# Performance work log

Hardware: AMD Instinct MI355X
Metric: run time of the kernel (lower is better)

The kernel has to match this reference:

```python
import jax, jax.numpy as jnp
import numpy as np
import math

N_HEADS = 16
D_EMB = 1024
D_HEAD = D_EMB // N_HEADS


def setup_inputs() -> dict:
    key = jax.random.key(0)
    ks = jax.random.split(key, 5)
    scale_in = 1.0 / math.sqrt(D_EMB)
    x = jax.random.normal(ks[0], (2, 2048, D_EMB), dtype=jnp.float32)
    w_in = jax.random.uniform(ks[1], (3 * D_EMB, D_EMB), dtype=jnp.float32, minval=-scale_in, maxval=scale_in)
    b_in = jax.random.uniform(ks[2], (3 * D_EMB,), dtype=jnp.float32, minval=-scale_in, maxval=scale_in)
    w_out = jax.random.uniform(ks[3], (D_EMB, D_EMB), dtype=jnp.float32, minval=-scale_in, maxval=scale_in)
    b_out = jax.random.uniform(ks[4], (D_EMB,), dtype=jnp.float32, minval=-scale_in, maxval=scale_in)
    return {"x": x, "w_in": w_in, "b_in": b_in, "w_out": w_out, "b_out": b_out, "apply_mask": 1}


def reference(x, w_in, b_in, w_out, b_out, apply_mask):
    B, S, D = x.shape
    # fused QKV projection: torch Linear uses y = x @ W^T + b
    qkv = jnp.einsum('bsd,ed->bse', x, w_in) + b_in  # [B,S,3D]
    q, k, v = jnp.split(qkv, 3, axis=-1)
    # [B,H,S,Dh]
    q = q.reshape(B, S, N_HEADS, D_HEAD).transpose(0, 2, 1, 3)
    k = k.reshape(B, S, N_HEADS, D_HEAD).transpose(0, 2, 1, 3)
    v = v.reshape(B, S, N_HEADS, D_HEAD).transpose(0, 2, 1, 3)
    w = jnp.einsum('bhqd,bhkd->bhqk', q, k)  # [B,H,S,S]
    if apply_mask:
        causal = jnp.triu(jnp.ones((S, S), dtype=bool), k=1)
        w = jnp.where(causal, -jnp.inf, w)
    w = w / jnp.sqrt(jnp.float32(D_HEAD)).astype(w.dtype)
    w = jax.nn.softmax(w, axis=-1)
    score = jnp.einsum('bhqk,bhkd->bhqd', w, v)  # [B,H,S,Dh]
    score = score.transpose(0, 2, 1, 3).reshape(B, S, D)
    return jnp.einsum('bsd,ed->bse', score, w_out) + b_out
```

## Files before the change

kernel.cpp:

```cpp
#include <hip/hip_runtime.h>
#include <stdint.h>

#define DEMB 1024
#define NHEAD 16
#define DHEAD 64
#define SEQ 2048
#define MROWS 4096

typedef __bf16 bf16x8 __attribute__((ext_vector_type(8)));
typedef float f32x4 __attribute__((ext_vector_type(4)));
typedef unsigned short u16;

#define LOG2E 1.44269504088896340736f

__device__ __forceinline__ u16 f2b(float f) {
  return __builtin_bit_cast(u16, (__bf16)f);
}
__device__ __forceinline__ uint32_t pk2(float a, float b) {
  return (uint32_t)f2b(a) | ((uint32_t)f2b(b) << 16);
}

__device__ __forceinline__ f32x4 mfma16(bf16x8 a, bf16x8 b, f32x4 c) {
  return __builtin_amdgcn_mfma_f32_16x16x32_bf16(a, b, c, 0, 0, 0);
}

__device__ __forceinline__ void gload_lds16(const void* g, void* l) {
  __builtin_amdgcn_global_load_lds(
      (__attribute__((address_space(1))) unsigned int*)(g),
      (__attribute__((address_space(3))) unsigned int*)(l), 16, 0, 0);
}

__device__ __forceinline__ void tile_barrier() {
  __builtin_amdgcn_sched_barrier(0);
  asm volatile("s_waitcnt vmcnt(0) lgkmcnt(0)" ::: "memory");
  __builtin_amdgcn_s_barrier();
  __builtin_amdgcn_sched_barrier(0);
}

__global__ void cvt3_f32_bf16(const float* __restrict__ a, int na,
                              const float* __restrict__ b, int nb,
                              const float* __restrict__ c, int nc,
                              u16* __restrict__ da, u16* __restrict__ db,
                              u16* __restrict__ dc) {
  const int total = (na + nb + nc) >> 2;
  const int stride = gridDim.x * blockDim.x;
  for (int t = blockIdx.x * blockDim.x + threadIdx.x; t < total; t += stride) {
    int i = t << 2;
    const float* s;
    u16* d;
    if (i < na) {
      s = a + i; d = da + i;
    } else if (i < na + nb) {
      s = b + (i - na); d = db + (i - na);
    } else {
      s = c + (i - na - nb); d = dc + (i - na - nb);
    }
    float4 f = *(const float4*)s;
    ushort4 o;
    o.x = f2b(f.x); o.y = f2b(f.y); o.z = f2b(f.z); o.w = f2b(f.w);
    *(ushort4*)d = o;
  }
}

template <int EPI>
__global__ __launch_bounds__(256, 2) void gemm_nt(
    const u16* __restrict__ A, const u16* __restrict__ Bw,
    const float* __restrict__ bias, int K, int N,
    u16* __restrict__ q_out, u16* __restrict__ k_out, u16* __restrict__ v_out,
    float* __restrict__ f_out) {
  __shared__ __align__(16) u16 As[128 * 64];
  __shared__ __align__(16) u16 Bs[128 * 64];
  const int tid = threadIdx.x;
  const int w = tid >> 6;
  const int lane = tid & 63;
  const int wm = w >> 1, wn = w & 1;
  const int m0 = blockIdx.y * 128, n0 = blockIdx.x * 128;
  const int l16 = lane & 15, lg = lane >> 4;
  const int st_row = lane >> 3, st_slot = lane & 7;

  f32x4 acc[4][4] = {};

  for (int k0 = 0; k0 < K; k0 += 64) {
#pragma unroll
    for (int i = 0; i < 4; ++i) {
      const int chunk = (w << 2) | i;
      const int row = (chunk << 3) | st_row;
      const int scol = (st_slot ^ (row & 7)) << 3;
      gload_lds16(A + (size_t)(m0 + row) * K + k0 + scol, (char*)As + (chunk << 10));
      gload_lds16(Bw + (size_t)(n0 + row) * K + k0 + scol, (char*)Bs + (chunk << 10));
    }
    __syncthreads();
#pragma unroll
    for (int ks = 0; ks < 2; ++ks) {
      bf16x8 af[4], bfr[4];
#pragma unroll
      for (int mi = 0; mi < 4; ++mi) {
        const int row = wm * 64 + mi * 16 + l16;
        const int cb = ((ks << 6) | (lg << 4)) ^ ((row & 7) << 4);
        af[mi] = *(const bf16x8*)((const char*)As + row * 128 + cb);
      }
#pragma unroll
      for (int ni = 0; ni < 4; ++ni) {
        const int row = wn * 64 + ni * 16 + l16;
        const int cb = ((ks << 6) | (lg << 4)) ^ ((row & 7) << 4);
        bfr[ni] = *(const bf16x8*)((const char*)Bs + row * 128 + cb);
      }
#pragma unroll
      for (int mi = 0; mi < 4; ++mi)
#pragma unroll
        for (int ni = 0; ni < 4; ++ni)
          acc[mi][ni] = mfma16(af[mi], bfr[ni], acc[mi][ni]);
    }
    __syncthreads();
  }

#pragma unroll
  for (int ni = 0; ni < 4; ++ni) {
    const int n = n0 + wn * 64 + ni * 16 + l16;
    const float bv = bias[n];
    if (EPI == 0) {
      const int part = n >> 10;
      const int hh = (n >> 6) & 15;
      const int dh = n & 63;
      if (part == 2) {
#pragma unroll
        for (int mi = 0; mi < 4; ++mi) {
          const int mbase = m0 + wm * 64 + mi * 16 + (lg << 2);
          const int bq = mbase >> 11, s0 = mbase & 2047;
          ushort4 o;
          o.x = f2b(acc[mi][ni][0] + bv);
          o.y = f2b(acc[mi][ni][1] + bv);
          o.z = f2b(acc[mi][ni][2] + bv);
          o.w = f2b(acc[mi][ni][3] + bv);
          *(ushort4*)(v_out + ((size_t)(((bq << 4) | hh) * 64 + dh)) * SEQ + s0) = o;
        }
      } else {
        const float scl = (part == 0) ? (0.125f * LOG2E) : 1.0f;
        u16* dst = (part == 0) ? q_out : k_out;
#pragma unroll
        for (int mi = 0; mi < 4; ++mi) {
#pragma unroll
          for (int i = 0; i < 4; ++i) {
            const int m = m0 + wm * 64 + mi * 16 + (lg << 2) + i;
            const int bq = m >> 11, s = m & 2047;
            dst[((size_t)((bq << 4) | hh) * SEQ + s) * DHEAD + dh] = f2b((acc[mi][ni][i] + bv) * scl);
          }
        }
      }
    } else {
#pragma unroll
      for (int mi = 0; mi < 4; ++mi)
#pragma unroll
        for (int i = 0; i < 4; ++i) {
          const int m = m0 + wm * 64 + mi * 16 + (lg << 2) + i;
          f_out[(size_t)m * N + n] = acc[mi][ni][i] + bv;
        }
    }
  }
}

__device__ __forceinline__ int swz4(int r) { return (r ^ (r >> 3)) & 15; }

__device__ __forceinline__ void stage_k(const u16* __restrict__ Kb, size_t base,
                                        int jt, u16* Ks, int w, int lane) {
#pragma unroll
  for (int i = 0; i < 4; ++i) {
    const int g = (w << 2) | i;
    const int row = (g << 2) | (lane >> 4);
    const int shat = (lane & 15) ^ swz4(row);
    const int kv = (row << 1) | (shat >> 3);
    const int del = (shat & 7) << 3;
    gload_lds16(Kb + base + (size_t)(jt * 128 + kv) * DHEAD + del,
                (char*)Ks + (g << 10));
  }
}

__device__ __forceinline__ void stage_v(const u16* __restrict__ VTg, size_t base,
                                        int jt, u16* Vs, int w, int lane) {
#pragma unroll
  for (int i = 0; i < 4; ++i) {
    const int g = (w << 2) | i;
    const int row = (g << 2) | (lane >> 4);
    const int shat = (lane & 15) ^ swz4(row);
    gload_lds16(VTg + base + (size_t)row * SEQ + jt * 128 + (shat << 3),
                (char*)Vs + (g << 10));
  }
}

__global__ __launch_bounds__(256, 2) void attn_fwd(
    const u16* __restrict__ Qb, const u16* __restrict__ Kb,
    const u16* __restrict__ VTg, u16* __restrict__ Ob,
    const int* __restrict__ amask) {
  __shared__ __align__(16) u16 Ks[2][64 * 128];
  __shared__ __align__(16) u16 Vt[2][64 * 128];
  __shared__ __align__(16) uint32_t Ps[4][1024];
  const int tid = threadIdx.x;
  const int w = tid >> 6, lane = tid & 63;
  const int l16 = lane & 15, lg = lane >> 4;

  const int id = blockIdx.x;
  const int xcd = id & 7;
  const int r = id >> 3;
  const int bh = (xcd << 2) | (r & 3);
  const int p = r >> 2;
  const int qiA = 31 - p, qiB = p;

  const size_t base = (size_t)bh * (SEQ * DHEAD);
  const bool causal = (amask[0] != 0);
  const int ntA = causal ? ((qiA >> 1) + 1) : (SEQ / 128);
  const int ntB = causal ? ((qiB >> 1) + 1) : (SEQ / 128);
  const int nt = ntA + ntB;
  const int b = bh >> 4, h = bh & 15;

  int qseg0 = qiA * 64;

  bf16x8 qf[2];
  {
    const u16* qp = Qb + base + (size_t)(qseg0 + (w << 4) + l16) * DHEAD + (lg << 3);
    qf[0] = *(const bf16x8*)qp;
    qf[1] = *(const bf16x8*)(qp + 32);
  }

  float mrow = -1e30f, lrowp = 0.f;
  f32x4 oacc[4] = {};

  const int key = (l16 & 7) << 2;
  char* prow = (char*)(&Ps[w][0]) + l16 * 256;

  stage_k(Kb, base, 0, Ks[0], w, lane);
  stage_v(VTg, base, 0, Vt[0], w, lane);
  tile_barrier();

  int cur = 0;
  for (int t = 0; t < nt; ++t) {
    const int j = (t >= ntA) ? (t - ntA) : t;
    const u16* Kcur = Ks[cur];
    const u16* Vcur = Vt[cur];
    const bool pre = (t + 1 < nt);
    const int jn = (t + 1 >= ntA) ? (t + 1 - ntA) : (t + 1);
    if (pre) stage_k(Kb, base, jn, Ks[cur ^ 1], w, lane);

    f32x4 sv[8];
    __builtin_amdgcn_s_setprio(1);
#pragma unroll
    for (int nf = 0; nf < 8; ++nf) {
      const int row2 = (nf << 3) | (l16 >> 1);
      const int sz = swz4(row2);
      const int s0 = ((l16 & 1) << 3) | lg;
      bf16x8 kf0 = *(const bf16x8*)((const char*)Kcur + row2 * 256 + ((s0 ^ sz) << 4));
      bf16x8 kf1 = *(const bf16x8*)((const char*)Kcur + row2 * 256 + (((s0 | 4) ^ sz) << 4));
      f32x4 s = {};
      s = mfma16(kf0, qf[0], s);
      s = mfma16(kf1, qf[1], s);
      sv[nf] = s;
    }
    __builtin_amdgcn_s_setprio(0);

    const bool segEnd = (t == ntA - 1) || (t == nt - 1);
    if (causal && segEnd) {
      const int q = qseg0 + (w << 4) + l16;
#pragma unroll
      for (int nf = 0; nf < 8; ++nf)
#pragma unroll
        for (int i = 0; i < 4; ++i) {
          const int kv = j * 128 + (nf << 4) + (lg << 2) + i;
          if (kv > q) sv[nf][i] = -1e30f;
        }
    }

    float tmaxg;
    {
      f32x4 mt;
#pragma unroll
      for (int i = 0; i < 4; ++i) {
        const float a01 = fmaxf(sv[0][i], sv[1][i]);
        const float a23 = fmaxf(sv[2][i], sv[3][i]);
        const float a45 = fmaxf(sv[4][i], sv[5][i]);
        const float a67 = fmaxf(sv[6][i], sv[7][i]);
        mt[i] = fmaxf(fmaxf(a01, a23), fmaxf(a45, a67));
      }
      tmaxg = fmaxf(fmaxf(mt[0], mt[1]), fmaxf(mt[2], mt[3]));
      tmaxg = fmaxf(tmaxg, __shfl_xor(tmaxg, 16));
      tmaxg = fmaxf(tmaxg, __shfl_xor(tmaxg, 32));
    }

    if (__any(tmaxg > mrow + 8.0f)) {
      const float mnew = fmaxf(mrow, tmaxg);
      const float corr = __builtin_amdgcn_exp2f(mrow - mnew);
      lrowp *= corr;
#pragma unroll
      for (int df = 0; df < 4; ++df)
#pragma unroll
        for (int i = 0; i < 4; ++i) oacc[df][i] *= corr;
      mrow = mnew;
    }

#pragma unroll
    for (int nf = 0; nf < 8; ++nf) {
      const float p0 = __builtin_amdgcn_exp2f(sv[nf][0] - mrow);
      const float p1 = __builtin_amdgcn_exp2f(sv[nf][1] - mrow);
      const float p2 = __builtin_amdgcn_exp2f(sv[nf][2] - mrow);
      const float p3 = __builtin_amdgcn_exp2f(sv[nf][3] - mrow);
      lrowp += (p0 + p1) + (p2 + p3);
      uint2 pkv;
      pkv.x = pk2(p0, p1);
      pkv.y = pk2(p2, p3);
      const int word = ((nf << 3) | (lg << 1)) ^ key;
      *(uint2*)(prow + word * 4) = pkv;
    }

    if (pre) stage_v(VTg, base, jn, Vt[cur ^ 1], w, lane);

    bf16x8 pa[4];
#pragma unroll
    for (int s = 0; s < 4; ++s)
      pa[s] = *(const bf16x8*)(prow + ((((s << 4) | (lg << 2)) ^ key) << 2));

    __builtin_amdgcn_s_setprio(1);
#pragma unroll
    for (int df = 0; df < 4; ++df) {
      const int row = (df << 4) + l16;
      const int sz = swz4(row) << 4;
#pragma unroll
      for (int s = 0; s < 4; ++s) {
        bf16x8 vf = *(const bf16x8*)((const char*)Vcur + row * 256 + (((s << 6) | (lg << 4)) ^ sz));
        oacc[df] = mfma16(vf, pa[s], oacc[df]);
      }
    }
    __builtin_amdgcn_s_setprio(0);

    if (segEnd) {
      float lrow = lrowp + __shfl_xor(lrowp, 16);
      lrow += __shfl_xor(lrow, 32);
      const float inv = 1.0f / lrow;
      const int s = qseg0 + (w << 4) + l16;
      u16* orow = Ob + (size_t)(b * SEQ + s) * DEMB + h * DHEAD;
#pragma unroll
      for (int df = 0; df < 4; ++df) {
        ushort4 o;
        o.x = f2b(oacc[df][0] * inv);
        o.y = f2b(oacc[df][1] * inv);
        o.z = f2b(oacc[df][2] * inv);
        o.w = f2b(oacc[df][3] * inv);
        *(ushort4*)(orow + (df << 4) + (lg << 2)) = o;
      }
      if (t != nt - 1) {
        qseg0 = qiB * 64;
        mrow = -1e30f;
        lrowp = 0.f;
#pragma unroll
        for (int df = 0; df < 4; ++df)
#pragma unroll
          for (int i = 0; i < 4; ++i) oacc[df][i] = 0.f;
        const u16* qp = Qb + base + (size_t)(qseg0 + (w << 4) + l16) * DHEAD + (lg << 3);
        qf[0] = *(const bf16x8*)qp;
        qf[1] = *(const bf16x8*)(qp + 32);
      }
    }

    if (pre) tile_barrier();
    cur ^= 1;
  }
}

extern "C" void kernel_launch(void* const* d_in, const int* in_sizes, int n_in,
                              void* d_out, int out_size, void* d_ws, size_t ws_size,
                              hipStream_t stream) {
  const float* x = (const float*)d_in[0];
  const float* w_in = (const float*)d_in[1];
  const float* b_in = (const float*)d_in[2];
  const float* w_out = (const float*)d_in[3];
  const float* b_out = (const float*)d_in[4];
  const int* amask = (const int*)d_in[5];
  float* out = (float*)d_out;

  u16* xb = (u16*)d_ws;
  u16* wib = xb + (size_t)MROWS * DEMB;
  u16* wob = wib + (size_t)3 * DEMB * DEMB;
  u16* Qb = wob + (size_t)DEMB * DEMB;
  u16* Kb = Qb + (size_t)MROWS * DEMB;
  u16* Vtg = Kb + (size_t)MROWS * DEMB;
  u16* Ab = xb;

  cvt3_f32_bf16<<<2048, 256, 0, stream>>>(x, MROWS * DEMB, w_in, 3 * DEMB * DEMB,
                                          w_out, DEMB * DEMB, xb, wib, wob);

  gemm_nt<0><<<dim3(24, 32), 256, 0, stream>>>(xb, wib, b_in, DEMB, 3 * DEMB,
                                               Qb, Kb, Vtg, nullptr);
  attn_fwd<<<512, 256, 0, stream>>>(Qb, Kb, Vtg, Ab, amask);
  gemm_nt<1><<<dim3(8, 32), 256, 0, stream>>>(Ab, wob, b_out, DEMB, DEMB,
                                              nullptr, nullptr, nullptr, out);
}
```

Baseline: 103.6 us.

## Double-buffer LDS tiles in the projection GEMM and use plain syncthreads in attention

The NT GEMM now keeps two LDS buffers for the A and B tiles. It issues the global-to-LDS loads for the next K-tile before running the MFMAs on the current tile, so global memory latency can overlap compute instead of stalling at a barrier every iteration. The attention kernel's custom tile_barrier (sched_barrier plus explicit waitcnt plus s_barrier) is replaced by __syncthreads. This doubles GEMM LDS use to 64 KB per block, which may squeeze occupancy, and it relies on __syncthreads waiting for the outstanding LDS-direct loads.

```diff
diff --git a/kernel.cpp b/kernel.cpp
--- a/kernel.cpp
+++ b/kernel.cpp
@@ -28,13 +28,6 @@
   __builtin_amdgcn_global_load_lds(
       (__attribute__((address_space(1))) unsigned int*)(g),
       (__attribute__((address_space(3))) unsigned int*)(l), 16, 0, 0);
-}
-
-__device__ __forceinline__ void tile_barrier() {
-  __builtin_amdgcn_sched_barrier(0);
-  asm volatile("s_waitcnt vmcnt(0) lgkmcnt(0)" ::: "memory");
-  __builtin_amdgcn_s_barrier();
-  __builtin_amdgcn_sched_barrier(0);
 }
 
 __global__ void cvt3_f32_bf16(const float* __restrict__ a, int na,
@@ -68,8 +61,8 @@
     const float* __restrict__ bias, int K, int N,
     u16* __restrict__ q_out, u16* __restrict__ k_out, u16* __restrict__ v_out,
     float* __restrict__ f_out) {
-  __shared__ __align__(16) u16 As[128 * 64];
-  __shared__ __align__(16) u16 Bs[128 * 64];
+  __shared__ __align__(16) u16 As[2][128 * 64];
+  __shared__ __align__(16) u16 Bs[2][128 * 64];
   const int tid = threadIdx.x;
   const int w = tid >> 6;
   const int lane = tid & 63;
@@ -80,16 +73,26 @@
 
   f32x4 acc[4][4] = {};
 
-  for (int k0 = 0; k0 < K; k0 += 64) {
+  auto stage = [&](int k0, int buf) {
 #pragma unroll
     for (int i = 0; i < 4; ++i) {
       const int chunk = (w << 2) | i;
       const int row = (chunk << 3) | st_row;
       const int scol = (st_slot ^ (row & 7)) << 3;
-      gload_lds16(A + (size_t)(m0 + row) * K + k0 + scol, (char*)As + (chunk << 10));
-      gload_lds16(Bw + (size_t)(n0 + row) * K + k0 + scol, (char*)Bs + (chunk << 10));
-    }
-    __syncthreads();
+      gload_lds16(A + (size_t)(m0 + row) * K + k0 + scol,
+                  (char*)As[buf] + (chunk << 10));
+      gload_lds16(Bw + (size_t)(n0 + row) * K + k0 + scol,
+                  (char*)Bs[buf] + (chunk << 10));
+    }
+  };
+
+  stage(0, 0);
+  __syncthreads();
+
+  int cur = 0;
+  for (int k0 = 0; k0 < K; k0 += 64) {
+    const bool pre = (k0 + 64 < K);
+    if (pre) stage(k0 + 64, cur ^ 1);
 #pragma unroll
     for (int ks = 0; ks < 2; ++ks) {
       bf16x8 af[4], bfr[4];
@@ -97,13 +100,13 @@
       for (int mi = 0; mi < 4; ++mi) {
         const int row = wm * 64 + mi * 16 + l16;
         const int cb = ((ks << 6) | (lg << 4)) ^ ((row & 7) << 4);
-        af[mi] = *(const bf16x8*)((const char*)As + row * 128 + cb);
+        af[mi] = *(const bf16x8*)((const char*)As[cur] + row * 128 + cb);
       }
 #pragma unroll
       for (int ni = 0; ni < 4; ++ni) {
         const int row = wn * 64 + ni * 16 + l16;
         const int cb = ((ks << 6) | (lg << 4)) ^ ((row & 7) << 4);
-        bfr[ni] = *(const bf16x8*)((const char*)Bs + row * 128 + cb);
+        bfr[ni] = *(const bf16x8*)((const char*)Bs[cur] + row * 128 + cb);
       }
 #pragma unroll
       for (int mi = 0; mi < 4; ++mi)
@@ -111,7 +114,8 @@
         for (int ni = 0; ni < 4; ++ni)
           acc[mi][ni] = mfma16(af[mi], bfr[ni], acc[mi][ni]);
     }
-    __syncthreads();
+    if (pre) __syncthreads();
+    cur ^= 1;
   }
 
 #pragma unroll
@@ -229,7 +233,7 @@
 
   stage_k(Kb, base, 0, Ks[0], w, lane);
   stage_v(VTg, base, 0, Vt[0], w, lane);
-  tile_barrier();
+  __syncthreads();
 
   int cur = 0;
   for (int t = 0; t < nt; ++t) {
@@ -358,7 +362,7 @@
       }
     }
 
-    if (pre) tile_barrier();
+    if (pre) __syncthreads();
     cur ^= 1;
   }
 }
```

Result: slower. 114.4 us (+10.5%).
